# Kernel optimization log

Hardware: AMD Instinct MI355X
Metric: run time of the kernel (lower is better)

The kernel has to match this reference:

```python
import jax, jax.numpy as jnp
import numpy as np

B, H, N, D = 2, 16, 4096, 64
NUM_PROJS = 8
BLOCK_SIZE = 256
SAMPLE_SIZE = 256
SCALE = D ** -0.5  # default scale = dim ** -0.5


def _unit_hamming_distance_array(size_n):
    # Gray-code permutation so that adjacent hash buckets differ in one bit
    a = np.array([0, 1], dtype=np.int32)
    for _ in range(size_n - 1):
        a = np.concatenate([a, np.flip(a) + a.shape[0]])
    return a

_PERM = jnp.asarray(_unit_hamming_distance_array(NUM_PROJS))
_ENC = jnp.asarray(2 ** np.arange(NUM_PROJS, dtype=np.int32))  # [num_projs]


def lsh_hash(x, proj_dir):
    # x: [b,h,n,d], proj_dir: [d,r] -> bucket id per token: [b,h,n]
    proj = jnp.einsum('bhnd,dr->bhnr', x, proj_dir)
    bin_ids = jnp.sum((proj > 0).astype(jnp.int32) * _ENC, axis=-1)
    return _PERM[bin_ids]


def attn_lse(q, k, v, scale):
    # exact softmax attention returning output and log-sum-exp
    s = jnp.einsum('...md,...nd->...mn', q, k) * scale
    lse = jax.nn.logsumexp(s, axis=-1, keepdims=True)
    out = jnp.einsum('...mn,...nv->...mv', jnp.exp(s - lse), v)
    return out, lse


def gather_seq(x, idx):
    # gather along the sequence axis (axis=2); broadcasts over last dim
    return jnp.take_along_axis(x, idx[..., None], axis=2)


def add_self_attentions(attn1, lse1, attn2, lse2):
    # combine two un-normalized softmax attentions via their lse's
    c = jax.nn.sigmoid(lse1 - lse2)  # = 1/(1+exp(lse2-lse1))
    attn = c * attn1 + (1.0 - c) * attn2
    lse = jnp.logaddexp(lse1, lse2)
    return attn, lse


def setup_inputs() -> dict:
    key = jax.random.key(0)
    kq, kk, kv, kp, ks = jax.random.split(key, 5)
    return {
        'query': jax.random.normal(kq, (B, H, N, D), jnp.float32),
        'key': jax.random.normal(kk, (B, H, N, D), jnp.float32),
        'value': jax.random.normal(kv, (B, H, N, D), jnp.float32),
        'proj_dir': jax.random.normal(kp, (D, NUM_PROJS), jnp.float32),
        'sampled_set': jax.random.randint(ks, (B, H, SAMPLE_SIZE), 0, N, dtype=jnp.int32),
    }


def reference(query, key, value, proj_dir, sampled_set):
    # --- LSH bucketing + stable sort of queries/keys by bucket id ---
    q_idx = jnp.argsort(lsh_hash(query, proj_dir), axis=2, stable=True)
    k_idx = jnp.argsort(lsh_hash(key, proj_dir), axis=2, stable=True)
    q_idx_inv = jnp.argsort(q_idx, axis=2, stable=True)

    q_s = gather_seq(query, q_idx)
    k_s = gather_seq(key, k_idx)
    v_s = gather_seq(value, k_idx)

    # --- block-diagonal attention in sorted order ---
    nb = N // BLOCK_SIZE
    q_b = q_s.reshape(B, H, nb, BLOCK_SIZE, D)
    k_b = k_s.reshape(B, H, nb, BLOCK_SIZE, D)
    v_b = v_s.reshape(B, H, nb, BLOCK_SIZE, D)
    attn_blk, lse_blk = attn_lse(q_b, k_b, v_b, SCALE)
    attn_blk = attn_blk.reshape(B, H, N, D)
    lse_blk = lse_blk.reshape(B, H, N, 1)
    # un-sort back to original query order
    attn_blk = gather_seq(attn_blk, q_idx_inv)
    lse_blk = gather_seq(lse_blk, q_idx_inv)

    # --- uniformly sampled residual attention, importance-weighted ---
    k_sub = gather_seq(key, sampled_set)
    v_sub = gather_seq(value, sampled_set)
    attn_res, lse_res = attn_lse(query, k_sub, v_sub, SCALE)
    lse_res = lse_res + jnp.log(N / SAMPLE_SIZE)

    attn, lse = add_self_attentions(attn_blk, lse_blk, attn_res, lse_res)
    return attn
```

## Files before the change

kernel.cpp:

```cpp
#include <hip/hip_runtime.h>
#include <hip/hip_bf16.h>
#include <math.h>

#define BH_ 32
#define N_ 4096
#define D_ 64
#define SAMP_ 256
#define SCALE_ 0.125f
#define HPAD 68

typedef __attribute__((ext_vector_type(4))) float f32x4;
typedef __attribute__((ext_vector_type(8))) short bf16x8;
typedef __attribute__((ext_vector_type(4))) short bf16x4;

static __device__ __forceinline__ unsigned pack2(float a, float b) {
    union { __hip_bfloat162 h; unsigned u; } c;
    c.h = __float22bfloat162_rn(make_float2(a, b));
    return c.u;
}

static __device__ __forceinline__ bf16x8 cvt8(const float* p) {
    const f32x4 a = *(const f32x4*)p, b = *(const f32x4*)(p + 4);
    union { unsigned u[4]; bf16x8 v; } r;
    r.u[0] = pack2(a[0], a[1]); r.u[1] = pack2(a[2], a[3]);
    r.u[2] = pack2(b[0], b[1]); r.u[3] = pack2(b[2], b[3]);
    return r.v;
}

__global__ __launch_bounds__(128) void hash_kernel(
    const float* __restrict__ q, const float* __restrict__ k,
    const float* __restrict__ pd,
    unsigned char* __restrict__ qbuck, unsigned char* __restrict__ kbuck)
{
    extern __shared__ char smraw[];
    float*  Xs  = (float*)smraw;
    double* Pdl = (double*)(smraw + 128 * HPAD * 4);

    int tid = threadIdx.x;
    const float* src = blockIdx.y ? k : q;
    unsigned char* dst = blockIdx.y ? kbuck : qbuck;
    size_t tok0 = (size_t)blockIdx.x * 128;

    {
        int d = tid >> 1, r0 = (tid & 1) * 4;
#pragma unroll
        for (int j = 0; j < 4; ++j)
            Pdl[d * 8 + r0 + j] = (double)pd[d * 8 + r0 + j];
    }
    {
        const float4* src4 = (const float4*)(src + tok0 * D_);
        for (int i = tid; i < 128 * 16; i += 128) {
            int r = i >> 4, c = i & 15;
            *(float4*)&Xs[r * HPAD + c * 4] = src4[i];
        }
    }
    __syncthreads();

    float xr[64];
#pragma unroll
    for (int c = 0; c < 16; ++c)
        *(float4*)&xr[c * 4] = *(const float4*)&Xs[tid * HPAD + c * 4];

    double acc[8];
#pragma unroll
    for (int r = 0; r < 8; ++r) acc[r] = 0.0;
#pragma unroll
    for (int d = 0; d < 64; ++d) {
        double x = (double)xr[d];
        const double* pr = Pdl + d * 8;
#pragma unroll
        for (int r = 0; r < 8; ++r) acc[r] += x * pr[r];
    }
    int bin = 0;
#pragma unroll
    for (int r = 0; r < 8; ++r)
        if (acc[r] > 0.0) bin |= (1 << r);
    dst[tok0 + tid] = (unsigned char)(bin ^ (bin >> 1));
}

__global__ __launch_bounds__(64) void sort_kernel(
    const unsigned char* __restrict__ qbuck,
    const unsigned char* __restrict__ kbuck,
    int* __restrict__ q_idx, int* __restrict__ k_idx)
{
    __shared__ unsigned short hist[64][256];
    __shared__ unsigned int   binstart[256];
    __shared__ unsigned char  bl[N_];

    int bh = blockIdx.x;
    int tensor = blockIdx.y;
    const unsigned char* buck = (tensor ? kbuck : qbuck) + bh * N_;
    int* idx_out = (tensor ? k_idx : q_idx) + bh * N_;
    int t = threadIdx.x;

    for (int i = t; i < N_; i += 64) bl[i] = buck[i];
    for (int b = 0; b < 256; ++b) hist[t][b] = 0;
    __syncthreads();

    for (int u = 0; u < 64; ++u)
        hist[t][bl[t * 64 + u]]++;
    __syncthreads();

    for (int bb = 0; bb < 4; ++bb) {
        int b = t + bb * 64;
        unsigned int running = 0;
        for (int tt = 0; tt < 64; ++tt) {
            unsigned int c = hist[tt][b];
            hist[tt][b] = (unsigned short)running;
            running += c;
        }
        binstart[b] = running;
    }
    __syncthreads();
    if (t == 0) {
        unsigned int run = 0;
        for (int b = 0; b < 256; ++b) {
            unsigned int c = binstart[b];
            binstart[b] = run;
            run += c;
        }
    }
    __syncthreads();

    for (int u = 0; u < 64; ++u) {
        int tok = t * 64 + u;
        int b = bl[tok];
        int pos = (int)(binstart[b] + hist[t][b]);
        hist[t][b]++;
        idx_out[pos] = tok;
    }
}

__device__ __forceinline__ void attn_pass(
    const float* __restrict__ key, const float* __restrict__ value,
    const int* __restrict__ kidx, size_t base,
    short* Ksm, short* Vsm, unsigned vtr,
    const bf16x8 (&qf)[2][2], int ll, int lg,
    f32x4 (&o)[4][2], float (&lsum)[2])
{
    int tid = threadIdx.x;
#pragma unroll
    for (int mt = 0; mt < 2; ++mt) {
        lsum[mt] = 0.f;
#pragma unroll
        for (int dt = 0; dt < 4; ++dt) { f32x4 z = {0.f,0.f,0.f,0.f}; o[dt][mt] = z; }
    }

    for (int ck = 0; ck < 2; ++ck) {
        __syncthreads();
        {
            const int* kc = kidx + ck * 128;
            int kkey = kc[((tid >> 6) << 4) | ((tid >> 1) & 15)];
            const float* kp = key + (base + (size_t)kkey) * D_
                              + ((tid >> 5) & 1) * 32 + (tid & 1) * 16;
            *(bf16x8*)&Ksm[tid * 16]     = cvt8(kp);
            *(bf16x8*)&Ksm[tid * 16 + 8] = cvt8(kp + 8);
            int vkey = kc[((tid >> 4) << 2) | (tid & 3)];
            const float* vp = value + (base + (size_t)vkey) * D_
                              + ((tid >> 2) & 3) * 16;
            *(bf16x8*)&Vsm[tid * 16]     = cvt8(vp);
            *(bf16x8*)&Vsm[tid * 16 + 8] = cvt8(vp + 8);
        }
        __syncthreads();

#pragma unroll
        for (int ks2 = 0; ks2 < 4; ++ks2) {
            unsigned pbu[2][4];
#pragma unroll
            for (int t = 0; t < 2; ++t) {
                int kt = ks2 * 2 + t;
                f32x4 s0 = {0.f,0.f,0.f,0.f}, s1 = {0.f,0.f,0.f,0.f};
#pragma unroll
                for (int ks = 0; ks < 2; ++ks) {
                    bf16x8 a = *(const bf16x8*)&Ksm[kt * 1024 + ks * 512 + ll * 32 + lg * 8];
                    s0 = __builtin_amdgcn_mfma_f32_16x16x32_bf16(a, qf[0][ks], s0, 0, 0, 0);
                    s1 = __builtin_amdgcn_mfma_f32_16x16x32_bf16(a, qf[1][ks], s1, 0, 0, 0);
                }
                f32x4 e0, e1;
#pragma unroll
                for (int r = 0; r < 4; ++r) {
                    e0[r] = __expf(s0[r] * SCALE_);
                    e1[r] = __expf(s1[r] * SCALE_);
                }
                lsum[0] += (e0[0] + e0[1]) + (e0[2] + e0[3]);
                lsum[1] += (e1[0] + e1[1]) + (e1[2] + e1[3]);
                pbu[0][t*2]   = pack2(e0[0], e0[1]);
                pbu[0][t*2+1] = pack2(e0[2], e0[3]);
                pbu[1][t*2]   = pack2(e1[0], e1[1]);
                pbu[1][t*2+1] = pack2(e1[2], e1[3]);
            }
            bf16x8 pb0, pb1;
            { union { unsigned u[4]; bf16x8 v; } c;
              c.u[0]=pbu[0][0]; c.u[1]=pbu[0][1]; c.u[2]=pbu[0][2]; c.u[3]=pbu[0][3]; pb0=c.v; }
            { union { unsigned u[4]; bf16x8 v; } c;
              c.u[0]=pbu[1][0]; c.u[1]=pbu[1][1]; c.u[2]=pbu[1][2]; c.u[3]=pbu[1][3]; pb1=c.v; }

            bf16x4 tr[4][2];
#pragma unroll
            for (int dt = 0; dt < 4; ++dt) {
                asm volatile("ds_read_b64_tr_b16 %0, %1 offset:%2"
                             : "=v"(tr[dt][0]) : "v"(vtr), "i"(ks2 * 4096 + dt * 128));
                asm volatile("ds_read_b64_tr_b16 %0, %1 offset:%2"
                             : "=v"(tr[dt][1]) : "v"(vtr), "i"(ks2 * 4096 + dt * 128 + 2048));
            }
            asm volatile("s_waitcnt lgkmcnt(0)" ::: "memory");
            __builtin_amdgcn_sched_barrier(0);
#pragma unroll
            for (int dt = 0; dt < 4; ++dt) {
                union { bf16x4 h[2]; bf16x8 v; } va;
                va.h[0] = tr[dt][0]; va.h[1] = tr[dt][1];
                o[dt][0] = __builtin_amdgcn_mfma_f32_16x16x32_bf16(va.v, pb0, o[dt][0], 0, 0, 0);
                o[dt][1] = __builtin_amdgcn_mfma_f32_16x16x32_bf16(va.v, pb1, o[dt][1], 0, 0, 0);
            }
        }
    }

#pragma unroll
    for (int mt = 0; mt < 2; ++mt) {
        float v = lsum[mt];
        v += __shfl_xor(v, 16);
        v += __shfl_xor(v, 32);
        lsum[mt] = v;
    }
}

__global__ __launch_bounds__(512, 4) void fused_attn(
    const float* __restrict__ query, const float* __restrict__ key,
    const float* __restrict__ value, const int* __restrict__ q_idx,
    const int* __restrict__ k_idx, const int* __restrict__ sampled,
    float* __restrict__ out)
{
    __shared__ short Ksm[8192];
    __shared__ short Vsm[8192];
    int wg = blockIdx.x, bh = wg >> 4, blk = wg & 15;
    int tid = threadIdx.x, w = tid >> 6, l = tid & 63, lg = l >> 4, ll = l & 15;
    size_t base = (size_t)bh * N_;
    const int* qidx = q_idx + base + blk * 256 + w * 32;
    unsigned vtr = (unsigned)(unsigned long long)(void*)&Vsm[0] + lg * 512 + ll * 8;

    int qr[2]; bf16x8 qf[2][2];
#pragma unroll
    for (int mt = 0; mt < 2; ++mt) {
        qr[mt] = qidx[mt * 16 + ll];
        const float* qp = query + (base + (size_t)qr[mt]) * D_;
#pragma unroll
        for (int ks = 0; ks < 2; ++ks)
            qf[mt][ks] = cvt8(qp + ks * 32 + lg * 8);
    }

    f32x4 o1[4][2], o2[4][2]; float l1[2], l2[2];
    attn_pass(key, value, k_idx + base + blk * 256, base, Ksm, Vsm, vtr, qf, ll, lg, o1, l1);
    attn_pass(key, value, sampled + bh * SAMP_,     base, Ksm, Vsm, vtr, qf, ll, lg, o2, l2);

#pragma unroll
    for (int mt = 0; mt < 2; ++mt) {
        float dn = 1.f / (l1[mt] + 16.f * l2[mt]);
        float* orow = out + (base + (size_t)qr[mt]) * D_ + lg * 4;
#pragma unroll
        for (int dt = 0; dt < 4; ++dt) {
            f32x4 v = (o1[dt][mt] + 16.f * o2[dt][mt]) * dn;
            *(f32x4*)&orow[dt * 16] = v;
        }
    }
}

extern "C" void kernel_launch(void* const* d_in, const int* in_sizes, int n_in,
                              void* d_out, int out_size, void* d_ws, size_t ws_size,
                              hipStream_t stream)
{
    const float* query = (const float*)d_in[0];
    const float* key   = (const float*)d_in[1];
    const float* value = (const float*)d_in[2];
    const float* pd    = (const float*)d_in[3];
    const int*   samp  = (const int*)d_in[4];
    float* out = (float*)d_out;

    char* ws = (char*)d_ws;
    unsigned char* qbuck = (unsigned char*)ws;
    unsigned char* kbuck = qbuck + (size_t)BH_ * N_;
    int* q_idx = (int*)(ws + 262144);
    int* k_idx = (int*)(ws + 262144 + 524288);

    size_t hash_lds = 128 * HPAD * 4 + 512 * 8;
    hipLaunchKernelGGL(hash_kernel, dim3(BH_ * N_ / 128, 2), dim3(128),
                       hash_lds, stream, query, key, pd, qbuck, kbuck);
    hipLaunchKernelGGL(sort_kernel, dim3(BH_, 2), dim3(64), 0, stream,
                       qbuck, kbuck, q_idx, k_idx);
    hipLaunchKernelGGL(fused_attn, dim3(512), dim3(512), 0, stream,
                       query, key, value, q_idx, k_idx, samp, out);
}
```

Measured before the change: 87.31 us.

## Double-buffer K/V staging and merge both attention passes into one accumulator

```diff
diff --git a/kernel.cpp b/kernel.cpp
--- a/kernel.cpp
+++ b/kernel.cpp
@@ -7,6 +7,7 @@
 #define D_ 64
 #define SAMP_ 256
 #define SCALE_ 0.125f
+#define LOG16_ 2.7725887222397811f
 #define HPAD 68
 
 typedef __attribute__((ext_vector_type(4))) float f32x4;
@@ -19,12 +20,15 @@
     return c.u;
 }
 
-static __device__ __forceinline__ bf16x8 cvt8(const float* p) {
-    const f32x4 a = *(const f32x4*)p, b = *(const f32x4*)(p + 4);
+static __device__ __forceinline__ bf16x8 cvt8v(f32x4 a, f32x4 b) {
     union { unsigned u[4]; bf16x8 v; } r;
     r.u[0] = pack2(a[0], a[1]); r.u[1] = pack2(a[2], a[3]);
     r.u[2] = pack2(b[0], b[1]); r.u[3] = pack2(b[2], b[3]);
     return r.v;
+}
+
+static __device__ __forceinline__ bf16x8 cvt8(const float* p) {
+    return cvt8v(*(const f32x4*)p, *(const f32x4*)(p + 4));
 }
 
 __global__ __launch_bounds__(128) void hash_kernel(
@@ -93,8 +97,16 @@
     int* idx_out = (tensor ? k_idx : q_idx) + bh * N_;
     int t = threadIdx.x;
 
-    for (int i = t; i < N_; i += 64) bl[i] = buck[i];
-    for (int b = 0; b < 256; ++b) hist[t][b] = 0;
+    {
+        const uint4* b4 = (const uint4*)buck;
+        uint4* bl4 = (uint4*)bl;
+        for (int i = t; i < N_ / 16; i += 64) bl4[i] = b4[i];
+    }
+    {
+        uint4* h4 = (uint4*)&hist[t][0];
+#pragma unroll
+        for (int i = 0; i < 32; ++i) h4[i] = make_uint4(0, 0, 0, 0);
+    }
     __syncthreads();
 
     for (int u = 0; u < 64; ++u)
@@ -131,14 +143,126 @@
     }
 }
 
-__device__ __forceinline__ void attn_pass(
-    const float* __restrict__ key, const float* __restrict__ value,
-    const int* __restrict__ kidx, size_t base,
-    short* Ksm, short* Vsm, unsigned vtr,
+struct StageReg { f32x4 k0a, k0b, k1a, k1b, v0, v1, v2, v3; };
+
+static __device__ __forceinline__ void stage_load(
+    StageReg& s, const float* __restrict__ key, const float* __restrict__ value,
+    size_t base, int2 kk, int vk, int kd, int vd)
+{
+    const float* kp0 = key + (base + (size_t)kk.x) * D_ + kd;
+    const float* kp1 = key + (base + (size_t)kk.y) * D_ + kd;
+    s.k0a = *(const f32x4*)kp0;       s.k0b = *(const f32x4*)(kp0 + 4);
+    s.k1a = *(const f32x4*)kp1;       s.k1b = *(const f32x4*)(kp1 + 4);
+    const float* vp = value + (base + (size_t)vk) * D_ + vd;
+    s.v0 = *(const f32x4*)vp;         s.v1 = *(const f32x4*)(vp + 4);
+    s.v2 = *(const f32x4*)(vp + 8);   s.v3 = *(const f32x4*)(vp + 12);
+}
+
+static __device__ __forceinline__ void stage_write(
+    const StageReg& s, short* __restrict__ Ks, short* __restrict__ Vs, int tid)
+{
+    *(bf16x8*)&Ks[tid * 16]     = cvt8v(s.k0a, s.k0b);
+    *(bf16x8*)&Ks[tid * 16 + 8] = cvt8v(s.k1a, s.k1b);
+    *(bf16x8*)&Vs[tid * 16]     = cvt8v(s.v0, s.v1);
+    *(bf16x8*)&Vs[tid * 16 + 8] = cvt8v(s.v2, s.v3);
+}
+
+static __device__ __forceinline__ void compute_chunk(
+    const short* __restrict__ Ks, unsigned vtrc, float bias,
     const bf16x8 (&qf)[2][2], int ll, int lg,
     f32x4 (&o)[4][2], float (&lsum)[2])
 {
-    int tid = threadIdx.x;
+#pragma unroll
+    for (int ks2 = 0; ks2 < 4; ++ks2) {
+        unsigned pbu[2][4];
+#pragma unroll
+        for (int t = 0; t < 2; ++t) {
+            int kt = ks2 * 2 + t;
+            f32x4 s0 = {0.f,0.f,0.f,0.f}, s1 = {0.f,0.f,0.f,0.f};
+#pragma unroll
+            for (int ks = 0; ks < 2; ++ks) {
+                bf16x8 a = *(const bf16x8*)&Ks[kt * 1024 + ks * 512 + lg * 128 + ll * 8];
+                s0 = __builtin_amdgcn_mfma_f32_16x16x32_bf16(a, qf[0][ks], s0, 0, 0, 0);
+                s1 = __builtin_amdgcn_mfma_f32_16x16x32_bf16(a, qf[1][ks], s1, 0, 0, 0);
+            }
+            f32x4 e0, e1;
+#pragma unroll
+            for (int r = 0; r < 4; ++r) {
+                e0[r] = __expf(fmaf(s0[r], SCALE_, bias));
+                e1[r] = __expf(fmaf(s1[r], SCALE_, bias));
+            }
+            lsum[0] += (e0[0] + e0[1]) + (e0[2] + e0[3]);
+            lsum[1] += (e1[0] + e1[1]) + (e1[2] + e1[3]);
+            pbu[0][t*2]   = pack2(e0[0], e0[1]);
+            pbu[0][t*2+1] = pack2(e0[2], e0[3]);
+            pbu[1][t*2]   = pack2(e1[0], e1[1]);
+            pbu[1][t*2+1] = pack2(e1[2], e1[3]);
+        }
+        bf16x8 pb0, pb1;
+        { union { unsigned u[4]; bf16x8 v; } c;
+          c.u[0]=pbu[0][0]; c.u[1]=pbu[0][1]; c.u[2]=pbu[0][2]; c.u[3]=pbu[0][3]; pb0=c.v; }
+        { union { unsigned u[4]; bf16x8 v; } c;
+          c.u[0]=pbu[1][0]; c.u[1]=pbu[1][1]; c.u[2]=pbu[1][2]; c.u[3]=pbu[1][3]; pb1=c.v; }
+
+        bf16x4 tr[4][2];
+#pragma unroll
+        for (int dt = 0; dt < 4; ++dt) {
+            asm volatile("ds_read_b64_tr_b16 %0, %1 offset:%2"
+                         : "=v"(tr[dt][0]) : "v"(vtrc), "i"(ks2 * 4096 + dt * 128));
+            asm volatile("ds_read_b64_tr_b16 %0, %1 offset:%2"
+                         : "=v"(tr[dt][1]) : "v"(vtrc), "i"(ks2 * 4096 + dt * 128 + 2048));
+        }
+        asm volatile("s_waitcnt lgkmcnt(0)" ::: "memory");
+        __builtin_amdgcn_sched_barrier(0);
+#pragma unroll
+        for (int dt = 0; dt < 4; ++dt) {
+            union { bf16x4 h[2]; bf16x8 v; } va;
+            va.h[0] = tr[dt][0]; va.h[1] = tr[dt][1];
+            o[dt][0] = __builtin_amdgcn_mfma_f32_16x16x32_bf16(va.v, pb0, o[dt][0], 0, 0, 0);
+            o[dt][1] = __builtin_amdgcn_mfma_f32_16x16x32_bf16(va.v, pb1, o[dt][1], 0, 0, 0);
+        }
+    }
+}
+
+__global__ __launch_bounds__(512, 4) void fused_attn(
+    const float* __restrict__ query, const float* __restrict__ key,
+    const float* __restrict__ value, const int* __restrict__ q_idx,
+    const int* __restrict__ k_idx, const int* __restrict__ sampled,
+    float* __restrict__ out)
+{
+    __shared__ short Ksm[2][8192];
+    __shared__ short Vsm[2][8192];
+    int wg = blockIdx.x, bh = wg >> 4, blk = wg & 15;
+    int tid = threadIdx.x, w = tid >> 6, l = tid & 63, lg = l >> 4, ll = l & 15;
+    size_t base = (size_t)bh * N_;
+    const int* qidx = q_idx + base + blk * 256 + w * 32;
+
+    int s_kt = tid >> 6, s_ks = (tid >> 5) & 1, s_lg = (tid >> 3) & 3, s_llh = tid & 7;
+    int s_krow = s_kt * 16 + s_llh * 2;
+    int s_kd   = s_ks * 32 + s_lg * 8;
+    int s_vrow = ((tid >> 4) << 2) | (tid & 3);
+    int s_vd   = ((tid >> 2) & 3) * 16;
+
+    const int* kidxA = k_idx + base + blk * 256;
+    const int* kidxB = sampled + bh * SAMP_;
+    int2 kI0 = *(const int2*)&kidxA[s_krow];
+    int2 kI1 = *(const int2*)&kidxA[128 + s_krow];
+    int2 kI2 = *(const int2*)&kidxB[s_krow];
+    int2 kI3 = *(const int2*)&kidxB[128 + s_krow];
+    int  vI0 = kidxA[s_vrow],       vI1 = kidxA[128 + s_vrow];
+    int  vI2 = kidxB[s_vrow],       vI3 = kidxB[128 + s_vrow];
+
+    int qr[2]; bf16x8 qf[2][2];
+#pragma unroll
+    for (int mt = 0; mt < 2; ++mt) {
+        qr[mt] = qidx[mt * 16 + ll];
+        const float* qp = query + (base + (size_t)qr[mt]) * D_;
+#pragma unroll
+        for (int ks = 0; ks < 2; ++ks)
+            qf[mt][ks] = cvt8(qp + ks * 32 + lg * 8);
+    }
+
+    f32x4 o[4][2]; float lsum[2];
 #pragma unroll
     for (int mt = 0; mt < 2; ++mt) {
         lsum[mt] = 0.f;
@@ -146,74 +270,26 @@
         for (int dt = 0; dt < 4; ++dt) { f32x4 z = {0.f,0.f,0.f,0.f}; o[dt][mt] = z; }
     }
 
-    for (int ck = 0; ck < 2; ++ck) {
-        __syncthreads();
-        {
-            const int* kc = kidx + ck * 128;
-            int kkey = kc[((tid >> 6) << 4) | ((tid >> 1) & 15)];
-            const float* kp = key + (base + (size_t)kkey) * D_
-                              + ((tid >> 5) & 1) * 32 + (tid & 1) * 16;
-            *(bf16x8*)&Ksm[tid * 16]     = cvt8(kp);
-            *(bf16x8*)&Ksm[tid * 16 + 8] = cvt8(kp + 8);
-            int vkey = kc[((tid >> 4) << 2) | (tid & 3)];
-            const float* vp = value + (base + (size_t)vkey) * D_
-                              + ((tid >> 2) & 3) * 16;
-            *(bf16x8*)&Vsm[tid * 16]     = cvt8(vp);
-            *(bf16x8*)&Vsm[tid * 16 + 8] = cvt8(vp + 8);
-        }
-        __syncthreads();
-
-#pragma unroll
-        for (int ks2 = 0; ks2 < 4; ++ks2) {
-            unsigned pbu[2][4];
-#pragma unroll
-            for (int t = 0; t < 2; ++t) {
-                int kt = ks2 * 2 + t;
-                f32x4 s0 = {0.f,0.f,0.f,0.f}, s1 = {0.f,0.f,0.f,0.f};
-#pragma unroll
-                for (int ks = 0; ks < 2; ++ks) {
-                    bf16x8 a = *(const bf16x8*)&Ksm[kt * 1024 + ks * 512 + ll * 32 + lg * 8];
-                    s0 = __builtin_amdgcn_mfma_f32_16x16x32_bf16(a, qf[0][ks], s0, 0, 0, 0);
-                    s1 = __builtin_amdgcn_mfma_f32_16x16x32_bf16(a, qf[1][ks], s1, 0, 0, 0);
-                }
-                f32x4 e0, e1;
-#pragma unroll
-                for (int r = 0; r < 4; ++r) {
-                    e0[r] = __expf(s0[r] * SCALE_);
-                    e1[r] = __expf(s1[r] * SCALE_);
-                }
-                lsum[0] += (e0[0] + e0[1]) + (e0[2] + e0[3]);
-                lsum[1] += (e1[0] + e1[1]) + (e1[2] + e1[3]);
-                pbu[0][t*2]   = pack2(e0[0], e0[1]);
-                pbu[0][t*2+1] = pack2(e0[2], e0[3]);
-                pbu[1][t*2]   = pack2(e1[0], e1[1]);
-                pbu[1][t*2+1] = pack2(e1[2], e1[3]);
-            }
-            bf16x8 pb0, pb1;
-            { union { unsigned u[4]; bf16x8 v; } c;
-              c.u[0]=pbu[0][0]; c.u[1]=pbu[0][1]; c.u[2]=pbu[0][2]; c.u[3]=pbu[0][3]; pb0=c.v; }
-            { union { unsigned u[4]; bf16x8 v; } c;
-              c.u[0]=pbu[1][0]; c.u[1]=pbu[1][1]; c.u[2]=pbu[1][2]; c.u[3]=pbu[1][3]; pb1=c.v; }
-
-            bf16x4 tr[4][2];
-#pragma unroll
-            for (int dt = 0; dt < 4; ++dt) {
-                asm volatile("ds_read_b64_tr_b16 %0, %1 offset:%2"
-                             : "=v"(tr[dt][0]) : "v"(vtr), "i"(ks2 * 4096 + dt * 128));
-                asm volatile("ds_read_b64_tr_b16 %0, %1 offset:%2"
-                             : "=v"(tr[dt][1]) : "v"(vtr), "i"(ks2 * 4096 + dt * 128 + 2048));
-            }
-            asm volatile("s_waitcnt lgkmcnt(0)" ::: "memory");
-            __builtin_amdgcn_sched_barrier(0);
-#pragma unroll
-            for (int dt = 0; dt < 4; ++dt) {
-                union { bf16x4 h[2]; bf16x8 v; } va;
-                va.h[0] = tr[dt][0]; va.h[1] = tr[dt][1];
-                o[dt][0] = __builtin_amdgcn_mfma_f32_16x16x32_bf16(va.v, pb0, o[dt][0], 0, 0, 0);
-                o[dt][1] = __builtin_amdgcn_mfma_f32_16x16x32_bf16(va.v, pb1, o[dt][1], 0, 0, 0);
-            }
-        }
-    }
+    unsigned vtr0 = (unsigned)(unsigned long long)(void*)&Vsm[0][0] + lg * 512 + ll * 8;
+    unsigned vtr1 = vtr0 + 16384;
+
+    StageReg sr;
+    stage_load(sr, key, value, base, kI0, vI0, s_kd, s_vd);
+    stage_write(sr, &Ksm[0][0], &Vsm[0][0], tid);
+    stage_load(sr, key, value, base, kI1, vI1, s_kd, s_vd);
+    __syncthreads();
+    stage_write(sr, &Ksm[1][0], &Vsm[1][0], tid);
+    stage_load(sr, key, value, base, kI2, vI2, s_kd, s_vd);
+    compute_chunk(&Ksm[0][0], vtr0, 0.f, qf, ll, lg, o, lsum);
+    __syncthreads();
+    stage_write(sr, &Ksm[0][0], &Vsm[0][0], tid);
+    stage_load(sr, key, value, base, kI3, vI3, s_kd, s_vd);
+    compute_chunk(&Ksm[1][0], vtr1, 0.f, qf, ll, lg, o, lsum);
+    __syncthreads();
+    stage_write(sr, &Ksm[1][0], &Vsm[1][0], tid);
+    compute_chunk(&Ksm[0][0], vtr0, LOG16_, qf, ll, lg, o, lsum);
+    __syncthreads();
+    compute_chunk(&Ksm[1][0], vtr1, LOG16_, qf, ll, lg, o, lsum);
 
 #pragma unroll
     for (int mt = 0; mt < 2; ++mt) {
@@ -222,43 +298,14 @@
         v += __shfl_xor(v, 32);
         lsum[mt] = v;
     }
-}
-
-__global__ __launch_bounds__(512, 4) void fused_attn(
-    const float* __restrict__ query, const float* __restrict__ key,
-    const float* __restrict__ value, const int* __restrict__ q_idx,
-    const int* __restrict__ k_idx, const int* __restrict__ sampled,
-    float* __restrict__ out)
-{
-    __shared__ short Ksm[8192];
-    __shared__ short Vsm[8192];
-    int wg = blockIdx.x, bh = wg >> 4, blk = wg & 15;
-    int tid = threadIdx.x, w = tid >> 6, l = tid & 63, lg = l >> 4, ll = l & 15;
-    size_t base = (size_t)bh * N_;
-    const int* qidx = q_idx + base + blk * 256 + w * 32;
-    unsigned vtr = (unsigned)(unsigned long long)(void*)&Vsm[0] + lg * 512 + ll * 8;
-
-    int qr[2]; bf16x8 qf[2][2];
+
 #pragma unroll
     for (int mt = 0; mt < 2; ++mt) {
-        qr[mt] = qidx[mt * 16 + ll];
-        const float* qp = query + (base + (size_t)qr[mt]) * D_;
-#pragma unroll
-        for (int ks = 0; ks < 2; ++ks)
-            qf[mt][ks] = cvt8(qp + ks * 32 + lg * 8);
-    }
-
-    f32x4 o1[4][2], o2[4][2]; float l1[2], l2[2];
-    attn_pass(key, value, k_idx + base + blk * 256, base, Ksm, Vsm, vtr, qf, ll, lg, o1, l1);
-    attn_pass(key, value, sampled + bh * SAMP_,     base, Ksm, Vsm, vtr, qf, ll, lg, o2, l2);
-
-#pragma unroll
-    for (int mt = 0; mt < 2; ++mt) {
-        float dn = 1.f / (l1[mt] + 16.f * l2[mt]);
+        float dn = 1.f / lsum[mt];
         float* orow = out + (base + (size_t)qr[mt]) * D_ + lg * 4;
 #pragma unroll
         for (int dt = 0; dt < 4; ++dt) {
-            f32x4 v = (o1[dt][mt] + 16.f * o2[dt][mt]) * dn;
+            f32x4 v = o[dt][mt] * dn;
             *(f32x4*)&orow[dt * 16] = v;
         }
     }
```

New measurement: 84.99 us. 1.03x faster.

## Widen sort and attention workgroups, merge attention passes into one accumulator

Applied to the files above, without the earlier changes.

```diff
diff --git a/kernel.cpp b/kernel.cpp
--- a/kernel.cpp
+++ b/kernel.cpp
@@ -7,6 +7,7 @@
 #define D_ 64
 #define SAMP_ 256
 #define SCALE_ 0.125f
+#define LOG16_ 2.7725887222397811f
 #define HPAD 68
 
 typedef __attribute__((ext_vector_type(4))) float f32x4;
@@ -19,14 +20,17 @@
     return c.u;
 }
 
-static __device__ __forceinline__ bf16x8 cvt8(const float* p) {
-    const f32x4 a = *(const f32x4*)p, b = *(const f32x4*)(p + 4);
+static __device__ __forceinline__ bf16x8 cvt8v(f32x4 a, f32x4 b) {
     union { unsigned u[4]; bf16x8 v; } r;
     r.u[0] = pack2(a[0], a[1]); r.u[1] = pack2(a[2], a[3]);
     r.u[2] = pack2(b[0], b[1]); r.u[3] = pack2(b[2], b[3]);
     return r.v;
 }
 
+static __device__ __forceinline__ bf16x8 cvt8(const float* p) {
+    return cvt8v(*(const f32x4*)p, *(const f32x4*)(p + 4));
+}
+
 __global__ __launch_bounds__(128) void hash_kernel(
     const float* __restrict__ q, const float* __restrict__ k,
     const float* __restrict__ pd,
@@ -78,153 +82,119 @@
     dst[tok0 + tid] = (unsigned char)(bin ^ (bin >> 1));
 }
 
-__global__ __launch_bounds__(64) void sort_kernel(
+__global__ __launch_bounds__(256) void sort_kernel(
     const unsigned char* __restrict__ qbuck,
     const unsigned char* __restrict__ kbuck,
     int* __restrict__ q_idx, int* __restrict__ k_idx)
 {
     __shared__ unsigned short hist[64][256];
     __shared__ unsigned int   binstart[256];
-    __shared__ unsigned char  bl[N_];
-
-    int bh = blockIdx.x;
-    int tensor = blockIdx.y;
+    __shared__ alignas(16) unsigned char bl[N_];
+
+    int bh = blockIdx.x, tensor = blockIdx.y;
     const unsigned char* buck = (tensor ? kbuck : qbuck) + bh * N_;
     int* idx_out = (tensor ? k_idx : q_idx) + bh * N_;
     int t = threadIdx.x;
 
-    for (int i = t; i < N_; i += 64) bl[i] = buck[i];
-    for (int b = 0; b < 256; ++b) hist[t][b] = 0;
-    __syncthreads();
-
-    for (int u = 0; u < 64; ++u)
-        hist[t][bl[t * 64 + u]]++;
-    __syncthreads();
-
-    for (int bb = 0; bb < 4; ++bb) {
-        int b = t + bb * 64;
-        unsigned int running = 0;
+    ((uint4*)bl)[t] = ((const uint4*)buck)[t];
+    {
+        uint4* h4 = (uint4*)&hist[0][0];
+        for (int i = t; i < 2048; i += 256) h4[i] = make_uint4(0, 0, 0, 0);
+    }
+    __syncthreads();
+
+    if (t < 64) {
+        for (int u = 0; u < 64; ++u) hist[t][bl[t * 64 + u]]++;
+    }
+    __syncthreads();
+
+    {
+        unsigned run = 0;
         for (int tt = 0; tt < 64; ++tt) {
-            unsigned int c = hist[tt][b];
-            hist[tt][b] = (unsigned short)running;
-            running += c;
-        }
-        binstart[b] = running;
-    }
-    __syncthreads();
-    if (t == 0) {
-        unsigned int run = 0;
-        for (int b = 0; b < 256; ++b) {
-            unsigned int c = binstart[b];
-            binstart[b] = run;
+            unsigned c = hist[tt][t];
+            hist[tt][t] = (unsigned short)run;
             run += c;
         }
-    }
-    __syncthreads();
-
-    for (int u = 0; u < 64; ++u) {
-        int tok = t * 64 + u;
-        int b = bl[tok];
-        int pos = (int)(binstart[b] + hist[t][b]);
-        hist[t][b]++;
-        idx_out[pos] = tok;
-    }
-}
-
-__device__ __forceinline__ void attn_pass(
-    const float* __restrict__ key, const float* __restrict__ value,
-    const int* __restrict__ kidx, size_t base,
-    short* Ksm, short* Vsm, unsigned vtr,
-    const bf16x8 (&qf)[2][2], int ll, int lg,
-    f32x4 (&o)[4][2], float (&lsum)[2])
-{
-    int tid = threadIdx.x;
-#pragma unroll
-    for (int mt = 0; mt < 2; ++mt) {
-        lsum[mt] = 0.f;
-#pragma unroll
-        for (int dt = 0; dt < 4; ++dt) { f32x4 z = {0.f,0.f,0.f,0.f}; o[dt][mt] = z; }
-    }
-
-    for (int ck = 0; ck < 2; ++ck) {
-        __syncthreads();
-        {
-            const int* kc = kidx + ck * 128;
-            int kkey = kc[((tid >> 6) << 4) | ((tid >> 1) & 15)];
-            const float* kp = key + (base + (size_t)kkey) * D_
-                              + ((tid >> 5) & 1) * 32 + (tid & 1) * 16;
-            *(bf16x8*)&Ksm[tid * 16]     = cvt8(kp);
-            *(bf16x8*)&Ksm[tid * 16 + 8] = cvt8(kp + 8);
-            int vkey = kc[((tid >> 4) << 2) | (tid & 3)];
-            const float* vp = value + (base + (size_t)vkey) * D_
-                              + ((tid >> 2) & 3) * 16;
-            *(bf16x8*)&Vsm[tid * 16]     = cvt8(vp);
-            *(bf16x8*)&Vsm[tid * 16 + 8] = cvt8(vp + 8);
-        }
-        __syncthreads();
-
-#pragma unroll
-        for (int ks2 = 0; ks2 < 4; ++ks2) {
-            unsigned pbu[2][4];
-#pragma unroll
-            for (int t = 0; t < 2; ++t) {
-                int kt = ks2 * 2 + t;
-                f32x4 s0 = {0.f,0.f,0.f,0.f}, s1 = {0.f,0.f,0.f,0.f};
-#pragma unroll
-                for (int ks = 0; ks < 2; ++ks) {
-                    bf16x8 a = *(const bf16x8*)&Ksm[kt * 1024 + ks * 512 + ll * 32 + lg * 8];
-                    s0 = __builtin_amdgcn_mfma_f32_16x16x32_bf16(a, qf[0][ks], s0, 0, 0, 0);
-                    s1 = __builtin_amdgcn_mfma_f32_16x16x32_bf16(a, qf[1][ks], s1, 0, 0, 0);
-                }
-                f32x4 e0, e1;
-#pragma unroll
-                for (int r = 0; r < 4; ++r) {
-                    e0[r] = __expf(s0[r] * SCALE_);
-                    e1[r] = __expf(s1[r] * SCALE_);
-                }
-                lsum[0] += (e0[0] + e0[1]) + (e0[2] + e0[3]);
-                lsum[1] += (e1[0] + e1[1]) + (e1[2] + e1[3]);
-                pbu[0][t*2]   = pack2(e0[0], e0[1]);
-                pbu[0][t*2+1] = pack2(e0[2], e0[3]);
-                pbu[1][t*2]   = pack2(e1[0], e1[1]);
-                pbu[1][t*2+1] = pack2(e1[2], e1[3]);
+        binstart[t] = run;
+    }
+    __syncthreads();
+
+    if (t < 64) {
+        unsigned b0 = binstart[t*4], b1 = binstart[t*4+1],
+                 b2 = binstart[t*4+2], b3 = binstart[t*4+3];
+        unsigned s = b0 + b1 + b2 + b3, p = s;
+#pragma unroll
+        for (int d = 1; d < 64; d <<= 1) {
+            unsigned y = __shfl_up(p, d);
+            if (t >= d) p += y;
+        }
+        unsigned e = p - s;
+        binstart[t*4]   = e;
+        binstart[t*4+1] = e + b0;
+        binstart[t*4+2] = e + b0 + b1;
+        binstart[t*4+3] = e + b0 + b1 + b2;
+    }
+    __syncthreads();
+
+    if (t < 64) {
+        for (int u = 0; u < 64; ++u) {
+            int tok = t * 64 + u;
+            int b = bl[tok];
+            int pos = (int)(binstart[b] + hist[t][b]);
+            hist[t][b]++;
+            idx_out[pos] = tok;
+        }
+    }
+}
+
+static __device__ __forceinline__ void compute_chunk16(
+    const short* __restrict__ Ks, unsigned vtr, float bias,
+    const bf16x8 (&qf)[2], int ll, int lg,
+    f32x4 (&o)[4], float& lsum)
+{
+#pragma unroll
+    for (int ks2 = 0; ks2 < 4; ++ks2) {
+        unsigned pbu[4];
+#pragma unroll
+        for (int t = 0; t < 2; ++t) {
+            int kt = ks2 * 2 + t;
+            f32x4 s = {0.f, 0.f, 0.f, 0.f};
+#pragma unroll
+            for (int ks = 0; ks < 2; ++ks) {
+                bf16x8 a = *(const bf16x8*)&Ks[kt * 1024 + ks * 512 + lg * 128 + ll * 8];
+                s = __builtin_amdgcn_mfma_f32_16x16x32_bf16(a, qf[ks], s, 0, 0, 0);
             }
-            bf16x8 pb0, pb1;
-            { union { unsigned u[4]; bf16x8 v; } c;
-              c.u[0]=pbu[0][0]; c.u[1]=pbu[0][1]; c.u[2]=pbu[0][2]; c.u[3]=pbu[0][3]; pb0=c.v; }
-            { union { unsigned u[4]; bf16x8 v; } c;
-              c.u[0]=pbu[1][0]; c.u[1]=pbu[1][1]; c.u[2]=pbu[1][2]; c.u[3]=pbu[1][3]; pb1=c.v; }
-
-            bf16x4 tr[4][2];
-#pragma unroll
-            for (int dt = 0; dt < 4; ++dt) {
-                asm volatile("ds_read_b64_tr_b16 %0, %1 offset:%2"
-                             : "=v"(tr[dt][0]) : "v"(vtr), "i"(ks2 * 4096 + dt * 128));
-                asm volatile("ds_read_b64_tr_b16 %0, %1 offset:%2"
-                             : "=v"(tr[dt][1]) : "v"(vtr), "i"(ks2 * 4096 + dt * 128 + 2048));
-            }
-            asm volatile("s_waitcnt lgkmcnt(0)" ::: "memory");
-            __builtin_amdgcn_sched_barrier(0);
-#pragma unroll
-            for (int dt = 0; dt < 4; ++dt) {
-                union { bf16x4 h[2]; bf16x8 v; } va;
-                va.h[0] = tr[dt][0]; va.h[1] = tr[dt][1];
-                o[dt][0] = __builtin_amdgcn_mfma_f32_16x16x32_bf16(va.v, pb0, o[dt][0], 0, 0, 0);
-                o[dt][1] = __builtin_amdgcn_mfma_f32_16x16x32_bf16(va.v, pb1, o[dt][1], 0, 0, 0);
-            }
-        }
-    }
-
-#pragma unroll
-    for (int mt = 0; mt < 2; ++mt) {
-        float v = lsum[mt];
-        v += __shfl_xor(v, 16);
-        v += __shfl_xor(v, 32);
-        lsum[mt] = v;
-    }
-}
-
-__global__ __launch_bounds__(512, 4) void fused_attn(
+            f32x4 e;
+#pragma unroll
+            for (int r = 0; r < 4; ++r) e[r] = __expf(fmaf(s[r], SCALE_, bias));
+            lsum += (e[0] + e[1]) + (e[2] + e[3]);
+            pbu[t*2]   = pack2(e[0], e[1]);
+            pbu[t*2+1] = pack2(e[2], e[3]);
+        }
+        bf16x8 pb;
+        { union { unsigned u[4]; bf16x8 v; } c;
+          c.u[0]=pbu[0]; c.u[1]=pbu[1]; c.u[2]=pbu[2]; c.u[3]=pbu[3]; pb = c.v; }
+
+        bf16x4 tr[4][2];
+#pragma unroll
+        for (int dt = 0; dt < 4; ++dt) {
+            asm volatile("ds_read_b64_tr_b16 %0, %1 offset:%2"
+                         : "=v"(tr[dt][0]) : "v"(vtr), "i"(ks2 * 4096 + dt * 128));
+            asm volatile("ds_read_b64_tr_b16 %0, %1 offset:%2"
+                         : "=v"(tr[dt][1]) : "v"(vtr), "i"(ks2 * 4096 + dt * 128 + 2048));
+        }
+        asm volatile("s_waitcnt lgkmcnt(0)" ::: "memory");
+        __builtin_amdgcn_sched_barrier(0);
+#pragma unroll
+        for (int dt = 0; dt < 4; ++dt) {
+            union { bf16x4 h[2]; bf16x8 v; } va;
+            va.h[0] = tr[dt][0]; va.h[1] = tr[dt][1];
+            o[dt] = __builtin_amdgcn_mfma_f32_16x16x32_bf16(va.v, pb, o[dt], 0, 0, 0);
+        }
+    }
+}
+
+__global__ __launch_bounds__(1024, 8) void fused_attn(
     const float* __restrict__ query, const float* __restrict__ key,
     const float* __restrict__ value, const int* __restrict__ q_idx,
     const int* __restrict__ k_idx, const int* __restrict__ sampled,
@@ -235,32 +205,56 @@
     int wg = blockIdx.x, bh = wg >> 4, blk = wg & 15;
     int tid = threadIdx.x, w = tid >> 6, l = tid & 63, lg = l >> 4, ll = l & 15;
     size_t base = (size_t)bh * N_;
-    const int* qidx = q_idx + base + blk * 256 + w * 32;
+
+    int s_krow = ((tid >> 7) << 4) | (tid & 15);
+    int s_kd   = ((tid >> 6) & 1) * 32 + ((tid >> 4) & 3) * 8;
+    int s_vrow = ((tid >> 5) << 2) | ((tid >> 1) & 3);
+    int s_vd   = ((tid >> 3) & 3) * 16 + (tid & 1) * 8;
+
+    const int* kidxA = k_idx + base + blk * 256;
+    const int* kidxB = sampled + bh * SAMP_;
+    int kI0 = kidxA[s_krow], kI1 = kidxA[128 + s_krow];
+    int kI2 = kidxB[s_krow], kI3 = kidxB[128 + s_krow];
+    int vI0 = kidxA[s_vrow], vI1 = kidxA[128 + s_vrow];
+    int vI2 = kidxB[s_vrow], vI3 = kidxB[128 + s_vrow];
+
+    const int* qidx = q_idx + base + blk * 256 + w * 16;
+    int qr = qidx[ll];
+    const float* qp = query + (base + (size_t)qr) * D_ + lg * 8;
+    bf16x8 qf[2] = { cvt8(qp), cvt8(qp + 32) };
+
+    f32x4 o[4];
+#pragma unroll
+    for (int dt = 0; dt < 4; ++dt) { f32x4 z = {0.f,0.f,0.f,0.f}; o[dt] = z; }
+    float lsum = 0.f;
     unsigned vtr = (unsigned)(unsigned long long)(void*)&Vsm[0] + lg * 512 + ll * 8;
 
-    int qr[2]; bf16x8 qf[2][2];
-#pragma unroll
-    for (int mt = 0; mt < 2; ++mt) {
-        qr[mt] = qidx[mt * 16 + ll];
-        const float* qp = query + (base + (size_t)qr[mt]) * D_;
-#pragma unroll
-        for (int ks = 0; ks < 2; ++ks)
-            qf[mt][ks] = cvt8(qp + ks * 32 + lg * 8);
-    }
-
-    f32x4 o1[4][2], o2[4][2]; float l1[2], l2[2];
-    attn_pass(key, value, k_idx + base + blk * 256, base, Ksm, Vsm, vtr, qf, ll, lg, o1, l1);
-    attn_pass(key, value, sampled + bh * SAMP_,     base, Ksm, Vsm, vtr, qf, ll, lg, o2, l2);
-
-#pragma unroll
-    for (int mt = 0; mt < 2; ++mt) {
-        float dn = 1.f / (l1[mt] + 16.f * l2[mt]);
-        float* orow = out + (base + (size_t)qr[mt]) * D_ + lg * 4;
-#pragma unroll
-        for (int dt = 0; dt < 4; ++dt) {
-            f32x4 v = (o1[dt][mt] + 16.f * o2[dt][mt]) * dn;
-            *(f32x4*)&orow[dt * 16] = v;
-        }
+#define STAGE_(KI, VI) do { \
+        const float* kp_ = key   + (base + (size_t)(KI)) * D_ + s_kd; \
+        const float* vp_ = value + (base + (size_t)(VI)) * D_ + s_vd; \
+        bf16x8 kv_ = cvt8(kp_), vv_ = cvt8(vp_); \
+        *(bf16x8*)&Ksm[tid * 8] = kv_; \
+        *(bf16x8*)&Vsm[tid * 8] = vv_; } while (0)
+
+    STAGE_(kI0, vI0); __syncthreads();
+    compute_chunk16(Ksm, vtr, 0.f, qf, ll, lg, o, lsum);
+    __syncthreads(); STAGE_(kI1, vI1); __syncthreads();
+    compute_chunk16(Ksm, vtr, 0.f, qf, ll, lg, o, lsum);
+    __syncthreads(); STAGE_(kI2, vI2); __syncthreads();
+    compute_chunk16(Ksm, vtr, LOG16_, qf, ll, lg, o, lsum);
+    __syncthreads(); STAGE_(kI3, vI3); __syncthreads();
+    compute_chunk16(Ksm, vtr, LOG16_, qf, ll, lg, o, lsum);
+#undef STAGE_
+
+    lsum += __shfl_xor(lsum, 16);
+    lsum += __shfl_xor(lsum, 32);
+
+    float dn = 1.f / lsum;
+    float* orow = out + (base + (size_t)qr) * D_ + lg * 4;
+#pragma unroll
+    for (int dt = 0; dt < 4; ++dt) {
+        f32x4 v = o[dt] * dn;
+        *(f32x4*)&orow[dt * 16] = v;
     }
 }
 
@@ -284,8 +278,8 @@
     size_t hash_lds = 128 * HPAD * 4 + 512 * 8;
     hipLaunchKernelGGL(hash_kernel, dim3(BH_ * N_ / 128, 2), dim3(128),
                        hash_lds, stream, query, key, pd, qbuck, kbuck);
-    hipLaunchKernelGGL(sort_kernel, dim3(BH_, 2), dim3(64), 0, stream,
+    hipLaunchKernelGGL(sort_kernel, dim3(BH_, 2), dim3(256), 0, stream,
                        qbuck, kbuck, q_idx, k_idx);
-    hipLaunchKernelGGL(fused_attn, dim3(512), dim3(512), 0, stream,
+    hipLaunchKernelGGL(fused_attn, dim3(512), dim3(1024), 0, stream,
                        query, key, value, q_idx, k_idx, samp, out);
 }
```

After: 90.32 us. 3.5% more time.

## Pipeline K/V gathers with register prefetch and merge attention passes into one loop

Applied to the files above, without the earlier changes.

```diff
diff --git a/kernel.cpp b/kernel.cpp
--- a/kernel.cpp
+++ b/kernel.cpp
@@ -7,6 +7,7 @@
 #define D_ 64
 #define SAMP_ 256
 #define SCALE_ 0.125f
+#define LOG16_ 2.7725887222397811f
 #define HPAD 68
 
 typedef __attribute__((ext_vector_type(4))) float f32x4;
@@ -19,12 +20,15 @@
     return c.u;
 }
 
-static __device__ __forceinline__ bf16x8 cvt8(const float* p) {
-    const f32x4 a = *(const f32x4*)p, b = *(const f32x4*)(p + 4);
+static __device__ __forceinline__ bf16x8 cvt8v(f32x4 a, f32x4 b) {
     union { unsigned u[4]; bf16x8 v; } r;
     r.u[0] = pack2(a[0], a[1]); r.u[1] = pack2(a[2], a[3]);
     r.u[2] = pack2(b[0], b[1]); r.u[3] = pack2(b[2], b[3]);
     return r.v;
+}
+
+static __device__ __forceinline__ bf16x8 cvt8(const float* p) {
+    return cvt8v(*(const f32x4*)p, *(const f32x4*)(p + 4));
 }
 
 __global__ __launch_bounds__(128) void hash_kernel(
@@ -59,7 +63,7 @@
     float xr[64];
 #pragma unroll
     for (int c = 0; c < 16; ++c)
-        *(float4*)&xr[c * 4] = *(const float4*)&Xs[tid * HPAD + c * 4];
+        *(f32x4*)&xr[c * 4] = *(const f32x4*)&Xs[tid * HPAD + c * 4];
 
     double acc[8];
 #pragma unroll
@@ -78,109 +82,160 @@
     dst[tok0 + tid] = (unsigned char)(bin ^ (bin >> 1));
 }
 
-__global__ __launch_bounds__(64) void sort_kernel(
+__global__ __launch_bounds__(256) void sort_kernel(
     const unsigned char* __restrict__ qbuck,
     const unsigned char* __restrict__ kbuck,
     int* __restrict__ q_idx, int* __restrict__ k_idx)
 {
     __shared__ unsigned short hist[64][256];
     __shared__ unsigned int   binstart[256];
-    __shared__ unsigned char  bl[N_];
-
-    int bh = blockIdx.x;
-    int tensor = blockIdx.y;
+    __shared__ alignas(16) unsigned char bl[N_];
+
+    int bh = blockIdx.x, tensor = blockIdx.y;
     const unsigned char* buck = (tensor ? kbuck : qbuck) + bh * N_;
     int* idx_out = (tensor ? k_idx : q_idx) + bh * N_;
     int t = threadIdx.x;
 
-    for (int i = t; i < N_; i += 64) bl[i] = buck[i];
-    for (int b = 0; b < 256; ++b) hist[t][b] = 0;
-    __syncthreads();
-
-    for (int u = 0; u < 64; ++u)
-        hist[t][bl[t * 64 + u]]++;
-    __syncthreads();
-
-    for (int bb = 0; bb < 4; ++bb) {
-        int b = t + bb * 64;
-        unsigned int running = 0;
+    ((uint4*)bl)[t] = ((const uint4*)buck)[t];
+    {
+        uint4* h4 = (uint4*)&hist[0][0];
+        for (int i = t; i < 2048; i += 256) h4[i] = make_uint4(0, 0, 0, 0);
+    }
+    __syncthreads();
+
+    if (t < 64) {
+        for (int u = 0; u < 64; ++u) hist[t][bl[t * 64 + u]]++;
+    }
+    __syncthreads();
+
+    {
+        unsigned run = 0;
         for (int tt = 0; tt < 64; ++tt) {
-            unsigned int c = hist[tt][b];
-            hist[tt][b] = (unsigned short)running;
-            running += c;
-        }
-        binstart[b] = running;
-    }
-    __syncthreads();
-    if (t == 0) {
-        unsigned int run = 0;
-        for (int b = 0; b < 256; ++b) {
-            unsigned int c = binstart[b];
-            binstart[b] = run;
+            unsigned c = hist[tt][t];
+            hist[tt][t] = (unsigned short)run;
             run += c;
         }
-    }
-    __syncthreads();
-
-    for (int u = 0; u < 64; ++u) {
-        int tok = t * 64 + u;
-        int b = bl[tok];
-        int pos = (int)(binstart[b] + hist[t][b]);
-        hist[t][b]++;
-        idx_out[pos] = tok;
-    }
-}
-
-__device__ __forceinline__ void attn_pass(
-    const float* __restrict__ key, const float* __restrict__ value,
-    const int* __restrict__ kidx, size_t base,
-    short* Ksm, short* Vsm, unsigned vtr,
-    const bf16x8 (&qf)[2][2], int ll, int lg,
-    f32x4 (&o)[4][2], float (&lsum)[2])
+        binstart[t] = run;
+    }
+    __syncthreads();
+
+    if (t < 64) {
+        unsigned b0 = binstart[t*4], b1 = binstart[t*4+1],
+                 b2 = binstart[t*4+2], b3 = binstart[t*4+3];
+        unsigned s = b0 + b1 + b2 + b3, p = s;
+#pragma unroll
+        for (int d = 1; d < 64; d <<= 1) {
+            unsigned y = __shfl_up(p, d);
+            if (t >= d) p += y;
+        }
+        unsigned e = p - s;
+        binstart[t*4]   = e;
+        binstart[t*4+1] = e + b0;
+        binstart[t*4+2] = e + b0 + b1;
+        binstart[t*4+3] = e + b0 + b1 + b2;
+    }
+    __syncthreads();
+
+    if (t < 64) {
+        for (int u = 0; u < 64; ++u) {
+            int tok = t * 64 + u;
+            int b = bl[tok];
+            int pos = (int)(binstart[b] + hist[t][b]);
+            hist[t][b]++;
+            idx_out[pos] = tok;
+        }
+    }
+}
+
+__global__ __launch_bounds__(512, 4) void fused_attn(
+    const float* __restrict__ query, const float* __restrict__ key,
+    const float* __restrict__ value, const int* __restrict__ q_idx,
+    const int* __restrict__ k_idx, const int* __restrict__ sampled,
+    float* __restrict__ out)
 {
-    int tid = threadIdx.x;
+    __shared__ __align__(16) short Ksm[4096];
+    __shared__ __align__(16) short Vsm[4096];
+    int wg = blockIdx.x, bh = wg >> 4, blk = wg & 15;
+    int tid = threadIdx.x, w = tid >> 6, l = tid & 63, lg = l >> 4, ll = l & 15;
+    size_t base = (size_t)bh * N_;
+
+    int krow = tid >> 3, kd8 = tid & 7;
+    int kofs = (krow >> 4) * 1024 + (kd8 >> 2) * 512 + (kd8 & 3) * 128 + (krow & 15) * 8;
+    int i6 = tid >> 6, l6 = tid & 63;
+    int vrow = (i6 >> 2) * 32 + ((l6 >> 5) * 4 + ((l6 >> 1) & 3)) + (i6 & 3) * 8;
+    int vd   = (((l6 >> 3) & 3) * 2 + (l6 & 1)) * 8;
+
+    const int* kidxA = k_idx + base + blk * 256;
+    const int* kidxB = sampled + bh * SAMP_;
+
+    const int* qidx = q_idx + base + blk * 256 + w * 32;
+    int qr[2]; bf16x8 qf[2][2];
+#pragma unroll
+    for (int mt = 0; mt < 2; ++mt) {
+        qr[mt] = qidx[mt * 16 + ll];
+        const float* qp = query + (base + (size_t)qr[mt]) * D_;
+#pragma unroll
+        for (int ks = 0; ks < 2; ++ks)
+            qf[mt][ks] = cvt8(qp + ks * 32 + lg * 8);
+    }
+
+    f32x4 o[4][2]; float lsum[2];
 #pragma unroll
     for (int mt = 0; mt < 2; ++mt) {
         lsum[mt] = 0.f;
 #pragma unroll
         for (int dt = 0; dt < 4; ++dt) { f32x4 z = {0.f,0.f,0.f,0.f}; o[dt][mt] = z; }
     }
-
-    for (int ck = 0; ck < 2; ++ck) {
+    unsigned vtr = (unsigned)(unsigned long long)(void*)&Vsm[0] + lg * 512 + ll * 8;
+
+    int kI = kidxA[krow], vI = kidxA[vrow];
+    f32x4 pk0, pk1, pv0, pv1;
+    {
+        const float* kp_ = key + (base + (size_t)kI) * D_ + kd8 * 8;
+        pk0 = *(const f32x4*)kp_; pk1 = *(const f32x4*)(kp_ + 4);
+        const float* vp_ = value + (base + (size_t)vI) * D_ + vd;
+        pv0 = *(const f32x4*)vp_; pv1 = *(const f32x4*)(vp_ + 4);
+    }
+    int kIn = kidxA[64 + krow], vIn = kidxA[64 + vrow];
+
+    for (int c = 0; c < 8; ++c) {
+        *(bf16x8*)&Ksm[kofs]    = cvt8v(pk0, pk1);
+        *(bf16x8*)&Vsm[tid * 8] = cvt8v(pv0, pv1);
         __syncthreads();
-        {
-            const int* kc = kidx + ck * 128;
-            int kkey = kc[((tid >> 6) << 4) | ((tid >> 1) & 15)];
-            const float* kp = key + (base + (size_t)kkey) * D_
-                              + ((tid >> 5) & 1) * 32 + (tid & 1) * 16;
-            *(bf16x8*)&Ksm[tid * 16]     = cvt8(kp);
-            *(bf16x8*)&Ksm[tid * 16 + 8] = cvt8(kp + 8);
-            int vkey = kc[((tid >> 4) << 2) | (tid & 3)];
-            const float* vp = value + (base + (size_t)vkey) * D_
-                              + ((tid >> 2) & 3) * 16;
-            *(bf16x8*)&Vsm[tid * 16]     = cvt8(vp);
-            *(bf16x8*)&Vsm[tid * 16 + 8] = cvt8(vp + 8);
-        }
-        __syncthreads();
-
-#pragma unroll
-        for (int ks2 = 0; ks2 < 4; ++ks2) {
+
+        if (c < 7) {
+            const float* kp_ = key + (base + (size_t)kIn) * D_ + kd8 * 8;
+            pk0 = *(const f32x4*)kp_; pk1 = *(const f32x4*)(kp_ + 4);
+            const float* vp_ = value + (base + (size_t)vIn) * D_ + vd;
+            pv0 = *(const f32x4*)vp_; pv1 = *(const f32x4*)(vp_ + 4);
+            if (c < 6) {
+                const int* nx = (c + 2 < 4) ? (kidxA + (c + 2) * 64)
+                                            : (kidxB + (c - 2) * 64);
+                kIn = nx[krow]; vIn = nx[vrow];
+            }
+        }
+
+        float bias = (c < 4) ? 0.f : LOG16_;
+#pragma unroll
+        for (int ks2 = 0; ks2 < 2; ++ks2) {
             unsigned pbu[2][4];
+            __builtin_amdgcn_s_setprio(1);
 #pragma unroll
             for (int t = 0; t < 2; ++t) {
                 int kt = ks2 * 2 + t;
                 f32x4 s0 = {0.f,0.f,0.f,0.f}, s1 = {0.f,0.f,0.f,0.f};
 #pragma unroll
                 for (int ks = 0; ks < 2; ++ks) {
-                    bf16x8 a = *(const bf16x8*)&Ksm[kt * 1024 + ks * 512 + ll * 32 + lg * 8];
+                    bf16x8 a = *(const bf16x8*)&Ksm[kt * 1024 + ks * 512 + lg * 128 + ll * 8];
                     s0 = __builtin_amdgcn_mfma_f32_16x16x32_bf16(a, qf[0][ks], s0, 0, 0, 0);
                     s1 = __builtin_amdgcn_mfma_f32_16x16x32_bf16(a, qf[1][ks], s1, 0, 0, 0);
                 }
+                __builtin_amdgcn_s_setprio(0);
                 f32x4 e0, e1;
 #pragma unroll
                 for (int r = 0; r < 4; ++r) {
-                    e0[r] = __expf(s0[r] * SCALE_);
-                    e1[r] = __expf(s1[r] * SCALE_);
+                    e0[r] = __expf(fmaf(s0[r], SCALE_, bias));
+                    e1[r] = __expf(fmaf(s1[r], SCALE_, bias));
                 }
                 lsum[0] += (e0[0] + e0[1]) + (e0[2] + e0[3]);
                 lsum[1] += (e1[0] + e1[1]) + (e1[2] + e1[3]);
@@ -188,12 +243,13 @@
                 pbu[0][t*2+1] = pack2(e0[2], e0[3]);
                 pbu[1][t*2]   = pack2(e1[0], e1[1]);
                 pbu[1][t*2+1] = pack2(e1[2], e1[3]);
+                __builtin_amdgcn_s_setprio(1);
             }
             bf16x8 pb0, pb1;
-            { union { unsigned u[4]; bf16x8 v; } c;
-              c.u[0]=pbu[0][0]; c.u[1]=pbu[0][1]; c.u[2]=pbu[0][2]; c.u[3]=pbu[0][3]; pb0=c.v; }
-            { union { unsigned u[4]; bf16x8 v; } c;
-              c.u[0]=pbu[1][0]; c.u[1]=pbu[1][1]; c.u[2]=pbu[1][2]; c.u[3]=pbu[1][3]; pb1=c.v; }
+            { union { unsigned u[4]; bf16x8 v; } cc;
+              cc.u[0]=pbu[0][0]; cc.u[1]=pbu[0][1]; cc.u[2]=pbu[0][2]; cc.u[3]=pbu[0][3]; pb0=cc.v; }
+            { union { unsigned u[4]; bf16x8 v; } cc;
+              cc.u[0]=pbu[1][0]; cc.u[1]=pbu[1][1]; cc.u[2]=pbu[1][2]; cc.u[3]=pbu[1][3]; pb1=cc.v; }
 
             bf16x4 tr[4][2];
 #pragma unroll
@@ -212,7 +268,12 @@
                 o[dt][0] = __builtin_amdgcn_mfma_f32_16x16x32_bf16(va.v, pb0, o[dt][0], 0, 0, 0);
                 o[dt][1] = __builtin_amdgcn_mfma_f32_16x16x32_bf16(va.v, pb1, o[dt][1], 0, 0, 0);
             }
-        }
+            __builtin_amdgcn_s_setprio(0);
+        }
+
+        __builtin_amdgcn_sched_barrier(0);
+        __builtin_amdgcn_s_barrier();
+        __builtin_amdgcn_sched_barrier(0);
     }
 
 #pragma unroll
@@ -222,43 +283,13 @@
         v += __shfl_xor(v, 32);
         lsum[mt] = v;
     }
-}
-
-__global__ __launch_bounds__(512, 4) void fused_attn(
-    const float* __restrict__ query, const float* __restrict__ key,
-    const float* __restrict__ value, const int* __restrict__ q_idx,
-    const int* __restrict__ k_idx, const int* __restrict__ sampled,
-    float* __restrict__ out)
-{
-    __shared__ short Ksm[8192];
-    __shared__ short Vsm[8192];
-    int wg = blockIdx.x, bh = wg >> 4, blk = wg & 15;
-    int tid = threadIdx.x, w = tid >> 6, l = tid & 63, lg = l >> 4, ll = l & 15;
-    size_t base = (size_t)bh * N_;
-    const int* qidx = q_idx + base + blk * 256 + w * 32;
-    unsigned vtr = (unsigned)(unsigned long long)(void*)&Vsm[0] + lg * 512 + ll * 8;
-
-    int qr[2]; bf16x8 qf[2][2];
 #pragma unroll
     for (int mt = 0; mt < 2; ++mt) {
-        qr[mt] = qidx[mt * 16 + ll];
-        const float* qp = query + (base + (size_t)qr[mt]) * D_;
-#pragma unroll
-        for (int ks = 0; ks < 2; ++ks)
-            qf[mt][ks] = cvt8(qp + ks * 32 + lg * 8);
-    }
-
-    f32x4 o1[4][2], o2[4][2]; float l1[2], l2[2];
-    attn_pass(key, value, k_idx + base + blk * 256, base, Ksm, Vsm, vtr, qf, ll, lg, o1, l1);
-    attn_pass(key, value, sampled + bh * SAMP_,     base, Ksm, Vsm, vtr, qf, ll, lg, o2, l2);
-
-#pragma unroll
-    for (int mt = 0; mt < 2; ++mt) {
-        float dn = 1.f / (l1[mt] + 16.f * l2[mt]);
+        float dn = 1.f / lsum[mt];
         float* orow = out + (base + (size_t)qr[mt]) * D_ + lg * 4;
 #pragma unroll
         for (int dt = 0; dt < 4; ++dt) {
-            f32x4 v = (o1[dt][mt] + 16.f * o2[dt][mt]) * dn;
+            f32x4 v = o[dt][mt] * dn;
             *(f32x4*)&orow[dt * 16] = v;
         }
     }
@@ -284,7 +315,7 @@
     size_t hash_lds = 128 * HPAD * 4 + 512 * 8;
     hipLaunchKernelGGL(hash_kernel, dim3(BH_ * N_ / 128, 2), dim3(128),
                        hash_lds, stream, query, key, pd, qbuck, kbuck);
-    hipLaunchKernelGGL(sort_kernel, dim3(BH_, 2), dim3(64), 0, stream,
+    hipLaunchKernelGGL(sort_kernel, dim3(BH_, 2), dim3(256), 0, stream,
                        qbuck, kbuck, q_idx, k_idx);
     hipLaunchKernelGGL(fused_attn, dim3(512), dim3(512), 0, stream,
                        query, key, value, q_idx, k_idx, samp, out);
```

Result: faster. 82.93 us (-5.0%).
